# Kernel optimization log

Measured on AMD Instinct MI355X. Metric: run time of the kernel, lower is better.

Reference implementation:

```python
import jax, jax.numpy as jnp
import numpy as np

EMB = 128     # embedding_size
HEADS = 4     # n_heads
LAYERS = 2    # n_layers
T = 10        # number of graphs / timesteps (== window_size)
N = 20000     # nodes per graph
E = 320000    # edges per graph
B = 4096      # clf_nodes
WIN = 10      # window_size
NEG_SLOPE = 0.2


def setup_inputs() -> dict:
    key = jax.random.key(0)
    ks = jax.random.split(key, 26)
    p = lambda k, shape: 0.05 * jax.random.normal(k, shape, jnp.float32)
    inp = {
        "embeddings": jax.random.normal(ks[0], (T, N, EMB), jnp.float32),
        "edges": jax.random.randint(ks[1], (T, 2, E), 0, N),
        "node_type": jax.random.randint(ks[2], (T, N), 0, 4),
        "edge_type": jax.random.randint(ks[3], (T, E), 0, 4),
        "clf_neighbors": jax.random.randint(ks[4], (B,), 0, N),
        "clf_nodes": jax.random.randint(ks[5], (B,), 0, N),
        # branch 1 GAT stacks: lin weight [L, H*C, D], attention vecs [L, H, C], bias [L, H*C]
        "gat_W1": p(ks[6], (LAYERS, HEADS * EMB, EMB)),
        "gat_as1": p(ks[7], (LAYERS, HEADS, EMB)),
        "gat_ad1": p(ks[8], (LAYERS, HEADS, EMB)),
        "gat_b1": p(ks[9], (LAYERS, HEADS * EMB)),
        "lin_W1": p(ks[10], (LAYERS, EMB, HEADS * EMB)),
        "lin_b1": p(ks[11], (LAYERS, EMB)),
        # branch 2
        "gat_W2": p(ks[12], (LAYERS, HEADS * EMB, EMB)),
        "gat_as2": p(ks[13], (LAYERS, HEADS, EMB)),
        "gat_ad2": p(ks[14], (LAYERS, HEADS, EMB)),
        "gat_b2": p(ks[15], (LAYERS, HEADS * EMB)),
        "lin_W2": p(ks[16], (LAYERS, EMB, HEADS * EMB)),
        "lin_b2": p(ks[17], (LAYERS, EMB)),
        # head MLP (fc1 consumes flattened [window * 2*D])
        "fc1_W": p(ks[18], (EMB, 2 * EMB * WIN)),
        "fc1_b": p(ks[19], (EMB,)),
        "fc2_W": p(ks[20], (2, EMB)),
        "fc2_b": p(ks[21], (2,)),
    }
    return inp


def _gat(x, src, dst, W, a_s, a_d, b):
    """PyG-style GATConv (concat=True, self-loops already in src/dst, eval mode)."""
    n = x.shape[0]
    h = (x @ W.T).reshape(n, HEADS, EMB)                       # [N,H,C]
    logits = jax.nn.leaky_relu((h * a_s).sum(-1)[src] + (h * a_d).sum(-1)[dst], NEG_SLOPE)  # [Etot,H]
    logits = logits - jax.ops.segment_max(logits, dst, num_segments=n)[dst]
    ex = jnp.exp(logits)
    alpha = ex / jax.ops.segment_sum(ex, dst, num_segments=n)[dst]  # segment softmax over targets
    out = jax.ops.segment_sum(alpha[:, :, None] * h[src], dst, num_segments=n)  # [N,H,C]
    return out.reshape(n, HEADS * EMB) + b


def _branch(embeddings, edges, gW, gas, gad, gb, lW, lb):
    loops = jnp.arange(N)

    def step(carry, inputs):
        x, edge = inputs
        src = jnp.concatenate([edge[0], loops])  # add self loops (PyG default)
        dst = jnp.concatenate([edge[1], loops])
        for i in range(LAYERS):
            x = _gat(x, src, dst, gW[i], gas[i], gad[i], gb[i])
            x = jax.nn.relu(x @ lW[i].T + lb[i])
        return carry, x

    _, outs = jax.lax.scan(step, 0, (embeddings, edges))
    return outs  # [T,N,EMB]


def reference(embeddings, edges, node_type, edge_type, clf_neighbors, clf_nodes,
              gat_W1, gat_as1, gat_ad1, gat_b1, lin_W1, lin_b1,
              gat_W2, gat_as2, gat_ad2, gat_b2, lin_W2, lin_b2,
              fc1_W, fc1_b, fc2_W, fc2_b):
    o1 = _branch(embeddings, edges, gat_W1, gat_as1, gat_ad1, gat_b1, lin_W1, lin_b1)
    o2 = _branch(embeddings, edges, gat_W2, gat_as2, gat_ad2, gat_b2, lin_W2, lin_b2)
    # original prepends each graph's output -> reversed timestep order
    e1 = o1[::-1][:, clf_nodes].transpose(1, 0, 2)  # [B,T,EMB]
    e2 = o2[::-1][:, clf_nodes].transpose(1, 0, 2)
    temp = jnp.concatenate([e1, e2], axis=2)        # [B,T,2*EMB]
    # slen == window_size -> skip buffer is fully filled by temp
    flat = temp.reshape(temp.shape[0], WIN * 2 * EMB)
    h = jax.nn.relu(flat @ fc1_W.T + fc1_b)
    return jax.nn.relu(h @ fc2_W.T + fc2_b)        # [B,2]
```

## Files before the change

kernel.cpp:

```cpp
#include <hip/hip_runtime.h>
#include <cstdint>

#define NNODES 20000
#define NEDGES 320000
#define ETOT   340000
#define TSTEPS 10
#define BCLF   4096
#define EMB    128
#define HC     512
#define NEG_SLOPE 0.2f

#define NSB    64
#define SBSPAN 313
#define PCAP   6912
#define ECHUNK 2048
#define NCHUNKS ((NEDGES + ECHUNK - 1) / ECHUNK)
#define NSCHUNK ((NNODES + 255) / 256)
#define STAGECAP 7424

typedef _Float16 half_t;
typedef __attribute__((ext_vector_type(8))) _Float16 half8;
typedef __attribute__((ext_vector_type(4))) float floatx4;

__global__ void cvt_split_kernel(const float* __restrict__ in,
                                 half_t* __restrict__ hi, half_t* __restrict__ lo, long n4) {
    long i = (long)blockIdx.x * 256 + threadIdx.x;
    if (i >= n4) return;
    float4 v = *(const float4*)&in[i * 4];
    half_t h[4], l[4];
    h[0] = (half_t)v.x; l[0] = (half_t)(v.x - (float)h[0]);
    h[1] = (half_t)v.y; l[1] = (half_t)(v.y - (float)h[1]);
    h[2] = (half_t)v.z; l[2] = (half_t)(v.z - (float)h[2]);
    h[3] = (half_t)v.w; l[3] = (half_t)(v.w - (float)h[3]);
    *(unsigned long long*)&hi[i * 4] = *(unsigned long long*)h;
    *(unsigned long long*)&lo[i * 4] = *(unsigned long long*)l;
}

__global__ __launch_bounds__(256) void part64_kernel(const int* __restrict__ edges,
                                                     int* __restrict__ bcnt,
                                                     int* __restrict__ pairs) {
    int g = blockIdx.y;
    int c = blockIdx.x;
    __shared__ int hist[NSB], gbase[NSB], cur[NSB];
    if (threadIdx.x < NSB) hist[threadIdx.x] = 0;
    __syncthreads();
    const int* srcp = edges + (long)g * 2 * NEDGES;
    const int* dstp = srcp + NEDGES;
    int e0 = c * ECHUNK + threadIdx.x;
    int s[8], d[8], sb[8];
#pragma unroll
    for (int i = 0; i < 8; i++) {
        int e = e0 + i * 256;
        if (e < NEDGES) {
            s[i] = srcp[e];
            d[i] = dstp[e];
            sb[i] = (int)((unsigned)d[i] / (unsigned)SBSPAN);
            atomicAdd(&hist[sb[i]], 1);
        } else sb[i] = -1;
    }
    __syncthreads();
    if (threadIdx.x < NSB) {
        int h = hist[threadIdx.x];
        gbase[threadIdx.x] = h ? atomicAdd(&bcnt[g * NSB + threadIdx.x], h) : 0;
        cur[threadIdx.x] = 0;
    }
    __syncthreads();
#pragma unroll
    for (int i = 0; i < 8; i++) {
        if (sb[i] >= 0) {
            int pos = gbase[sb[i]] + atomicAdd(&cur[sb[i]], 1);
            int v = s[i] | ((d[i] - sb[i] * SBSPAN) << 15);
            pairs[((long)(g * NSB + sb[i])) * PCAP + pos] = v;
        }
    }
}

__global__ __launch_bounds__(256) void count_sb_kernel(const int* __restrict__ pairs,
                                                       const int* __restrict__ bcnt,
                                                       int* __restrict__ counts) {
    int g = blockIdx.x >> 6, sb = blockIdx.x & 63;
    __shared__ int hist[SBSPAN];
    for (int i = threadIdx.x; i < SBSPAN; i += 256) hist[i] = 0;
    __syncthreads();
    int n0 = sb * SBSPAN;
    int cnt = bcnt[g * NSB + sb];
    const int* p = pairs + (long)(g * NSB + sb) * PCAP;
    for (int k = threadIdx.x; k < cnt; k += 256)
        atomicAdd(&hist[p[k] >> 15], 1);
    __syncthreads();
    int nn = min(SBSPAN, NNODES - n0);
    for (int i = threadIdx.x; i < nn; i += 256)
        counts[g * NNODES + n0 + i] = hist[i];
}

__global__ void scanA_kernel(const int* __restrict__ counts, int* __restrict__ bsum) {
    int g = blockIdx.x / NSCHUNK, ch = blockIdx.x % NSCHUNK;
    int i = ch * 256 + threadIdx.x;
    int v = (i < NNODES) ? counts[g * NNODES + i] + 1 : 0;
    for (int off = 32; off; off >>= 1) v += __shfl_down(v, off);
    __shared__ int ws[4];
    if ((threadIdx.x & 63) == 0) ws[threadIdx.x >> 6] = v;
    __syncthreads();
    if (threadIdx.x == 0) bsum[blockIdx.x] = ws[0] + ws[1] + ws[2] + ws[3];
}

__global__ void scanB_kernel(const int* __restrict__ bsum, int* __restrict__ boff,
                             int* __restrict__ rowptr) {
    int g = blockIdx.x;
    int tid = threadIdx.x;
    int v = (tid < NSCHUNK) ? bsum[g * NSCHUNK + tid] : 0;
    __shared__ int buf[128];
    buf[tid] = v;
    __syncthreads();
    for (int off = 1; off < 128; off <<= 1) {
        int t = (tid >= off) ? buf[tid - off] : 0;
        __syncthreads();
        buf[tid] += t;
        __syncthreads();
    }
    if (tid < NSCHUNK) boff[g * NSCHUNK + tid] = buf[tid] - v;
    if (tid == 127) rowptr[g * (NNODES + 1) + NNODES] = buf[127];
}

__global__ void scanC_kernel(const int* __restrict__ counts, const int* __restrict__ boff,
                             int* __restrict__ rowptr) {
    int g = blockIdx.x / NSCHUNK, ch = blockIdx.x % NSCHUNK;
    int tid = threadIdx.x;
    int i = ch * 256 + tid;
    int v = (i < NNODES) ? counts[g * NNODES + i] + 1 : 0;
    __shared__ int buf[256];
    buf[tid] = v;
    __syncthreads();
    for (int off = 1; off < 256; off <<= 1) {
        int t = (tid >= off) ? buf[tid - off] : 0;
        __syncthreads();
        buf[tid] += t;
        __syncthreads();
    }
    int excl = boff[blockIdx.x] + buf[tid] - v;
    if (i < NNODES) rowptr[g * (NNODES + 1) + i] = excl;
}

__global__ __launch_bounds__(256) void fill_sb_kernel(const int* __restrict__ pairs,
                                                      const int* __restrict__ bcnt,
                                                      const int* __restrict__ rowptr,
                                                      int* __restrict__ csr_src) {
    int g = blockIdx.x >> 6, sb = blockIdx.x & 63;
    __shared__ int cur[SBSPAN];
    __shared__ int stage[STAGECAP];
    int n0 = sb * SBSPAN;
    int nn = min(SBSPAN, NNODES - n0);
    const int* rp = rowptr + g * (NNODES + 1);
    int base = rp[n0];
    int span = rp[n0 + nn] - base;
    for (int i = threadIdx.x; i < nn; i += 256) {
        int rb = rp[n0 + i] - base;
        stage[rb] = n0 + i;
        cur[i] = rb + 1;
    }
    __syncthreads();
    int cnt = bcnt[g * NSB + sb];
    const int* p = pairs + (long)(g * NSB + sb) * PCAP;
    for (int k = threadIdx.x; k < cnt; k += 256) {
        int v = p[k];
        int pos = atomicAdd(&cur[v >> 15], 1);
        stage[pos] = v & 0x7fff;
    }
    __syncthreads();
    int* dst = csr_src + (long)g * ETOT + base;
    for (int k = threadIdx.x; k < span; k += 256) dst[k] = stage[k];
}

__global__ void prep_was_kernel(const float* __restrict__ W1, const float* __restrict__ W2,
                                const float* __restrict__ as1, const float* __restrict__ as2,
                                const float* __restrict__ ad1, const float* __restrict__ ad2,
                                float* __restrict__ was, float* __restrict__ wad) {
    int b = blockIdx.x;
    int l = b >> 3, z = (b >> 2) & 1, h = b & 3;
    int k = threadIdx.x;
    const float* W  = z ? W2 : W1;
    const float* av = z ? as2 : as1;
    const float* dv = z ? ad2 : ad1;
    float s = 0.f, d = 0.f;
    for (int c = 0; c < 128; c++) {
        float w = W[(long)l * HC * EMB + (h * 128 + c) * 128 + k];
        s = fmaf(w, av[(l * 4 + h) * 128 + c], s);
        d = fmaf(w, dv[(l * 4 + h) * 128 + c], d);
    }
    long idx = ((l * 2 + z) * 4 + h) * 128 + k;
    was[idx] = s;
    wad[idx] = d;
}

__global__ void pack_ws_kernel(const float* __restrict__ wasb, const float* __restrict__ wadb,
                               half_t* __restrict__ WS0h, half_t* __restrict__ WS0l,
                               half_t* __restrict__ WS1h, half_t* __restrict__ WS1l) {
    int b = blockIdx.x;
    int k = threadIdx.x;
    if (b < 16) {
        int z = b >> 3, d = (b >> 2) & 1, h = b & 3;
        const float* src = d ? wadb : wasb;
        float v = src[((long)z * 4 + h) * 128 + k];
        half_t hi = (half_t)v;
        WS0h[b * 128 + k] = hi;
        WS0l[b * 128 + k] = (half_t)(v - (float)hi);
    } else {
        int b2 = b - 16;
        int z = b2 >> 4, r = b2 & 15;
        float v = 0.f;
        if (r < 8) {
            int d = r >> 2, h = r & 3;
            const float* src = d ? wadb : wasb;
            v = src[((long)(2 + z) * 4 + h) * 128 + k];
        }
        half_t hi = (half_t)v;
        WS1h[(z * 16 + r) * 128 + k] = hi;
        WS1l[(z * 16 + r) * 128 + k] = (half_t)(v - (float)hi);
    }
}

__global__ void prep_M_kernel(const float* __restrict__ gW1, const float* __restrict__ gW2,
                              const float* __restrict__ lW1, const float* __restrict__ lW2,
                              half_t* __restrict__ Mh, half_t* __restrict__ Ml) {
    int k = blockIdx.x;
    int inst = blockIdx.y;
    int l = inst >> 1, z = inst & 1;
    int c = threadIdx.x;
    const float* gW = (z ? gW2 : gW1) + (long)l * HC * EMB;
    const float* lW = (z ? lW2 : lW1) + (long)l * EMB * HC;
    float acc[4] = {0.f, 0.f, 0.f, 0.f};
    for (int cp = 0; cp < 128; cp++) {
#pragma unroll
        for (int h = 0; h < 4; h++) {
            float lw = lW[(long)k * 512 + h * 128 + cp];
            float gw = gW[(long)(h * 128 + cp) * 128 + c];
            acc[h] = fmaf(lw, gw, acc[h]);
        }
    }
#pragma unroll
    for (int h = 0; h < 4; h++) {
        long o = ((long)inst * 128 + k) * 512 + h * 128 + c;
        half_t hi = (half_t)acc[h];
        Mh[o] = hi;
        Ml[o] = (half_t)(acc[h] - (float)hi);
    }
}

__global__ void prep_cb_kernel(const float* __restrict__ lW1, const float* __restrict__ lW2,
                               const float* __restrict__ gb1_, const float* __restrict__ gb2_,
                               const float* __restrict__ lb1_, const float* __restrict__ lb2_,
                               float* __restrict__ cb) {
    int inst = blockIdx.x;
    int l = inst >> 1, z = inst & 1;
    int k = threadIdx.x;
    const float* lW = (z ? lW2 : lW1) + (long)l * EMB * HC;
    const float* gb = (z ? gb2_ : gb1_) + l * HC;
    const float* lb = (z ? lb2_ : lb1_) + l * EMB;
    float a = lb[k];
    for (int j = 0; j < 512; j++) a = fmaf(lW[(long)k * 512 + j], gb[j], a);
    cb[inst * 128 + k] = a;
}

__global__ __launch_bounds__(256) void scores_b(
    const half_t* __restrict__ Ahb, const half_t* __restrict__ Alb, long aInst,
    const half_t* __restrict__ WShb, const half_t* __restrict__ WSlb, long wInst, int wMask,
    float* __restrict__ outb, long oInst, int M, int OS, int CMAX) {
    int iy = blockIdx.y;
    const half_t* Ah = Ahb + (long)iy * aInst;
    const half_t* Al = Alb + (long)iy * aInst;
    const half_t* WSh = WShb + (long)(iy & wMask) * wInst;
    const half_t* WSl = WSlb + (long)(iy & wMask) * wInst;
    float* out = outb + (long)iy * oInst;
    __shared__ half_t Bh[16 * 128];
    __shared__ half_t Bl[16 * 128];
    int tid = threadIdx.x;
    *(half8*)&Bh[tid * 8] = *(const half8*)&WSh[tid * 8];
    *(half8*)&Bl[tid * 8] = *(const half8*)&WSl[tid * 8];
    __syncthreads();
    int wave = tid >> 6, lane = tid & 63;
    int l16 = lane & 15, chunk = lane >> 4;
    int r0 = blockIdx.x * 64 + wave * 16;
    int rowc = r0 + l16; if (rowc > M - 1) rowc = M - 1;
    floatx4 acc = (floatx4)0.f;
#pragma unroll
    for (int ko = 0; ko < 128; ko += 32) {
        half8 ah = *(const half8*)&Ah[(long)rowc * 128 + ko + chunk * 8];
        half8 al = *(const half8*)&Al[(long)rowc * 128 + ko + chunk * 8];
        half8 bh = *(const half8*)&Bh[l16 * 128 + ko + chunk * 8];
        half8 bl = *(const half8*)&Bl[l16 * 128 + ko + chunk * 8];
        acc = __builtin_amdgcn_mfma_f32_16x16x32_f16(ah, bh, acc, 0, 0, 0);
        acc = __builtin_amdgcn_mfma_f32_16x16x32_f16(ah, bl, acc, 0, 0, 0);
        acc = __builtin_amdgcn_mfma_f32_16x16x32_f16(al, bh, acc, 0, 0, 0);
    }
#pragma unroll
    for (int reg = 0; reg < 4; reg++) {
        int rr = r0 + chunk * 4 + reg;
        if (rr < M && l16 < CMAX) out[(long)rr * OS + l16] = acc[reg];
    }
}

__global__ __launch_bounds__(256) void agg_x_kernel(
    const half_t* __restrict__ Xb, long xsT, long xsG,
    const float* __restrict__ ssb, int stsh, long ssT, long ssG, int zcol,
    const int* __restrict__ rowptr, const int* __restrict__ csr_src,
    half_t* __restrict__ Yh, half_t* __restrict__ Yl, int t0) {
    int tz = blockIdx.z, t = t0 + tz, z = blockIdx.y;
    int gz = tz * 2 + z;
    int n = blockIdx.x * 4 + (threadIdx.x >> 6);
    int lane = threadIdx.x & 63;
    int h = lane >> 4, cg = lane & 15;
    const int* rp = rowptr + t * (NNODES + 1);
    int beg = rp[n], end = rp[n + 1];
    const int* cs = csr_src + (long)t * ETOT;
    const half_t* Xz = Xb + (long)t * xsT + (long)gz * xsG;
    const float* sz = ssb + (long)t * ssT + (long)gz * ssG + (long)z * zcol;
    float sd = sz[((long)n << stsh) + 4 + h];
    float acc[8];
#pragma unroll
    for (int c = 0; c < 8; c++) acc[c] = 0.f;
    float den = 0.f;
    int j = beg;
    for (; j + 4 <= end; j += 4) {
        int s0 = cs[j], s1 = cs[j + 1], s2 = cs[j + 2], s3 = cs[j + 3];
        float v0 = sz[((long)s0 << stsh) + h];
        float v1 = sz[((long)s1 << stsh) + h];
        float v2 = sz[((long)s2 << stsh) + h];
        float v3 = sz[((long)s3 << stsh) + h];
        half8 x0 = *(const half8*)&Xz[(long)s0 * 128 + cg * 8];
        half8 x1 = *(const half8*)&Xz[(long)s1 * 128 + cg * 8];
        half8 x2 = *(const half8*)&Xz[(long)s2 * 128 + cg * 8];
        half8 x3 = *(const half8*)&Xz[(long)s3 * 128 + cg * 8];
        float L0 = v0 + sd, L1 = v1 + sd, L2 = v2 + sd, L3 = v3 + sd;
        float w0 = __expf(fmaxf(L0, NEG_SLOPE * L0));
        float w1 = __expf(fmaxf(L1, NEG_SLOPE * L1));
        float w2 = __expf(fmaxf(L2, NEG_SLOPE * L2));
        float w3 = __expf(fmaxf(L3, NEG_SLOPE * L3));
        den += (w0 + w1) + (w2 + w3);
#pragma unroll
        for (int c = 0; c < 8; c++) {
            float a = acc[c];
            a = fmaf(w0, (float)x0[c], a);
            a = fmaf(w1, (float)x1[c], a);
            a = fmaf(w2, (float)x2[c], a);
            a = fmaf(w3, (float)x3[c], a);
            acc[c] = a;
        }
    }
    for (; j < end; j++) {
        int src = cs[j];
        float sv = sz[((long)src << stsh) + h];
        half8 x = *(const half8*)&Xz[(long)src * 128 + cg * 8];
        float L = sv + sd;
        float w = __expf(fmaxf(L, NEG_SLOPE * L));
        den += w;
#pragma unroll
        for (int c = 0; c < 8; c++) acc[c] = fmaf(w, (float)x[c], acc[c]);
    }
    float inv = 1.0f / den;
    half8 oh, ol;
#pragma unroll
    for (int c = 0; c < 8; c++) {
        float v = acc[c] * inv;
        half_t hi = (half_t)v;
        oh[c] = hi;
        ol[c] = (half_t)(v - (float)hi);
    }
    long yb = ((long)gz * NNODES + n) * 512 + h * 128 + cg * 8;
    *(half8*)&Yh[yb] = oh;
    *(half8*)&Yl[yb] = ol;
}

template <bool F32OUT>
__global__ __launch_bounds__(256) void gemm_b(
    const half_t* __restrict__ Ahb, const half_t* __restrict__ Alb, long aInst,
    const half_t* __restrict__ Bhb, const half_t* __restrict__ Blb, long bInst,
    const float* __restrict__ biasb, long biasInst,
    half_t* __restrict__ Ch, half_t* __restrict__ Cl, float* __restrict__ Cf,
    long cInst, int M, int N, int K) {
    const int i = blockIdx.z;
    const half_t* __restrict__ Ah = Ahb + (long)i * aInst;
    const half_t* __restrict__ Al = Alb + (long)i * aInst;
    const half_t* __restrict__ Bh = Bhb + (long)(i & 1) * bInst;
    const half_t* __restrict__ Bl = Blb + (long)(i & 1) * bInst;
    const float* __restrict__ bias = biasb + (long)(i & 1) * biasInst;

    __shared__ half_t Ash[4 * 128 * 8];
    __shared__ half_t Asl[4 * 128 * 8];
    __shared__ half_t Bsh[4 * 128 * 8];
    __shared__ half_t Bsl[4 * 128 * 8];

    const int tid = threadIdx.x;
    const int row0 = blockIdx.x * 128;
    const int col0 = blockIdx.y * 128;
    const int wave = tid >> 6;
    const int lane = tid & 63;
    const int wm = (wave >> 1) * 64;
    const int wn = (wave & 1) * 64;
    const int chunk = lane >> 4;
    const int l16 = lane & 15;

    floatx4 acc[4][4];
#pragma unroll
    for (int ii = 0; ii < 4; ii++)
#pragma unroll
        for (int j = 0; j < 4; j++) acc[ii][j] = (floatx4)0.0f;

    for (int k0 = 0; k0 < K; k0 += 32) {
        __syncthreads();
#pragma unroll
        for (int p = 0; p < 2; p++) {
            int idx = p * 256 + tid;
            int r = idx >> 2, kc = idx & 3;
            int arow = row0 + r;
            half8 vah, val;
            if (arow < M) {
                vah = *(const half8*)&Ah[(long)arow * K + k0 + kc * 8];
                val = *(const half8*)&Al[(long)arow * K + k0 + kc * 8];
            } else {
#pragma unroll
                for (int q = 0; q < 8; q++) { vah[q] = (half_t)0.f; val[q] = (half_t)0.f; }
            }
            *(half8*)&Ash[(kc * 128 + r) * 8] = vah;
            *(half8*)&Asl[(kc * 128 + r) * 8] = val;
            long boff = (long)(col0 + r) * K + k0 + kc * 8;
            *(half8*)&Bsh[(kc * 128 + r) * 8] = *(const half8*)&Bh[boff];
            *(half8*)&Bsl[(kc * 128 + r) * 8] = *(const half8*)&Bl[boff];
        }
        __syncthreads();
        half8 afh[4], afl[4], bfh[4], bfl[4];
#pragma unroll
        for (int mi = 0; mi < 4; mi++) {
            int o = (chunk * 128 + wm + mi * 16 + l16) * 8;
            afh[mi] = *(const half8*)&Ash[o];
            afl[mi] = *(const half8*)&Asl[o];
        }
#pragma unroll
        for (int ni = 0; ni < 4; ni++) {
            int o = (chunk * 128 + wn + ni * 16 + l16) * 8;
            bfh[ni] = *(const half8*)&Bsh[o];
            bfl[ni] = *(const half8*)&Bsl[o];
        }
#pragma unroll
        for (int mi = 0; mi < 4; mi++)
#pragma unroll
            for (int ni = 0; ni < 4; ni++) {
                acc[mi][ni] = __builtin_amdgcn_mfma_f32_16x16x32_f16(
                    afh[mi], bfh[ni], acc[mi][ni], 0, 0, 0);
                acc[mi][ni] = __builtin_amdgcn_mfma_f32_16x16x32_f16(
                    afh[mi], bfl[ni], acc[mi][ni], 0, 0, 0);
                acc[mi][ni] = __builtin_amdgcn_mfma_f32_16x16x32_f16(
                    afl[mi], bfh[ni], acc[mi][ni], 0, 0, 0);
            }
    }

    const int r4 = (lane >> 4) * 4;
#pragma unroll
    for (int mi = 0; mi < 4; mi++) {
#pragma unroll
        for (int reg = 0; reg < 4; reg++) {
            int row = row0 + wm + mi * 16 + r4 + reg;
            if (row >= M) continue;
#pragma unroll
            for (int ni = 0; ni < 4; ni++) {
                int col = col0 + wn + ni * 16 + l16;
                float v = fmaxf(acc[mi][ni][reg] + bias[col], 0.f);
                long o = (long)i * cInst + (long)row * N + col;
                if (F32OUT) {
                    Cf[o] = v;
                } else {
                    half_t hi = (half_t)v;
                    Ch[o] = hi;
                    Cl[o] = (half_t)(v - (float)hi);
                }
            }
        }
    }
}

__global__ void gather_kernel(const half_t* __restrict__ Xh, const half_t* __restrict__ Xl,
                              const int* __restrict__ clf,
                              half_t* __restrict__ flath, half_t* __restrict__ flatl, int t0) {
    int b = blockIdx.x;
    int z = blockIdx.y;
    int tz = blockIdx.z;
    int t = t0 + tz, gz = tz * 2 + z;
    int j = threadIdx.x;
    int node = clf[b];
    long dst = (long)b * (TSTEPS * 2 * EMB) + (TSTEPS - 1 - t) * (2 * EMB) + z * EMB;
    long src = ((long)gz * NNODES + node) * EMB;
    ((unsigned int*)&flath[dst])[j] = ((const unsigned int*)&Xh[src])[j];
    ((unsigned int*)&flatl[dst])[j] = ((const unsigned int*)&Xl[src])[j];
}

__global__ void fc2_kernel(const float* __restrict__ h1, const float* __restrict__ W,
                           const float* __restrict__ bias, float* __restrict__ out) {
    int row = blockIdx.x;
    int lane = threadIdx.x;
    float x0 = h1[(long)row * 128 + lane];
    float x1 = h1[(long)row * 128 + 64 + lane];
    float p0 = x0 * W[lane] + x1 * W[64 + lane];
    float p1 = x0 * W[128 + lane] + x1 * W[192 + lane];
    for (int off = 32; off; off >>= 1) {
        p0 += __shfl_down(p0, off);
        p1 += __shfl_down(p1, off);
    }
    if (lane == 0) {
        out[row * 2 + 0] = fmaxf(p0 + bias[0], 0.f);
        out[row * 2 + 1] = fmaxf(p1 + bias[1], 0.f);
    }
}

extern "C" void kernel_launch(void* const* d_in, const int* in_sizes, int n_in,
                              void* d_out, int out_size, void* d_ws, size_t ws_size,
                              hipStream_t stream) {
    const float* emb     = (const float*)d_in[0];
    const int*   edges   = (const int*)d_in[1];
    const int*   clf     = (const int*)d_in[5];
    const float* gat_W1  = (const float*)d_in[6];
    const float* gat_as1 = (const float*)d_in[7];
    const float* gat_ad1 = (const float*)d_in[8];
    const float* gat_b1  = (const float*)d_in[9];
    const float* lin_W1  = (const float*)d_in[10];
    const float* lin_b1  = (const float*)d_in[11];
    const float* gat_W2  = (const float*)d_in[12];
    const float* gat_as2 = (const float*)d_in[13];
    const float* gat_ad2 = (const float*)d_in[14];
    const float* gat_b2  = (const float*)d_in[15];
    const float* lin_W2  = (const float*)d_in[16];
    const float* lin_b2  = (const float*)d_in[17];
    const float* fc1_W   = (const float*)d_in[18];
    const float* fc1_b   = (const float*)d_in[19];
    const float* fc2_W   = (const float*)d_in[20];
    const float* fc2_b   = (const float*)d_in[21];
    float* out = (float*)d_out;

    char* ws = (char*)d_ws;
    size_t off = 0;
    auto alloc = [&](size_t bytes) -> char* {
        char* p = ws + off;
        off += (bytes + 255) & ~(size_t)255;
        return p;
    };
    int* counts  = (int*)alloc((size_t)TSTEPS * NNODES * 4);
    int* rowptr  = (int*)alloc((size_t)TSTEPS * (NNODES + 1) * 4);
    int* csr_src = (int*)alloc((size_t)TSTEPS * ETOT * 4);
    int* bsum    = (int*)alloc((size_t)TSTEPS * NSCHUNK * 4);
    int* boff    = (int*)alloc((size_t)TSTEPS * NSCHUNK * 4);
    int* bcnt    = (int*)alloc((size_t)TSTEPS * NSB * 4);
    half_t* embh = (half_t*)alloc((size_t)TSTEPS * NNODES * EMB * 2);
    half_t* Mh   = (half_t*)alloc((size_t)4 * EMB * HC * 2);
    half_t* Ml   = (half_t*)alloc((size_t)4 * EMB * HC * 2);
    float*  cb   = (float*)alloc((size_t)4 * EMB * 4);
    half_t* fc1Wh = (half_t*)alloc((size_t)EMB * 2 * EMB * TSTEPS * 2);
    half_t* fc1Wl = (half_t*)alloc((size_t)EMB * 2 * EMB * TSTEPS * 2);
    float* wasb = (float*)alloc((size_t)2 * 2 * 4 * 128 * 4);
    float* wadb = (float*)alloc((size_t)2 * 2 * 4 * 128 * 4);
    half_t* WS0h = (half_t*)alloc((size_t)16 * 128 * 2);
    half_t* WS0l = (half_t*)alloc((size_t)16 * 128 * 2);
    half_t* WS1h = (half_t*)alloc((size_t)2 * 16 * 128 * 2);
    half_t* WS1l = (half_t*)alloc((size_t)2 * 16 * 128 * 2);
    float* s0buf = (float*)alloc((size_t)TSTEPS * NNODES * 16 * 4);
    half_t* flath = (half_t*)alloc((size_t)BCLF * (TSTEPS * 2 * EMB) * 2);
    half_t* flatl = (half_t*)alloc((size_t)BCLF * (TSTEPS * 2 * EMB) * 2);
    float* h1buf = (float*)alloc((size_t)BCLF * EMB * 4);

    size_t region_base = off;
    half_t* embl = (half_t*)alloc((size_t)TSTEPS * NNODES * EMB * 2);
    int* pairs   = (int*)alloc((size_t)TSTEPS * NSB * PCAP * 4);

    const size_t perT = ((size_t)2 * NNODES * HC * 2 * 2) +
                        ((size_t)2 * NNODES * EMB * 2 * 2) +
                        ((size_t)2 * NNODES * 8 * 4) + 2048;
    int TG = 1;
    if (ws_size > region_base + perT) {
        size_t cap = (ws_size - region_base) / perT;
        TG = (cap >= 10) ? 10 : (int)cap;
        if (TG < 1) TG = 1;
    }
    off = region_base;
    half_t* Yh = (half_t*)alloc((size_t)TG * 2 * NNODES * HC * 2);
    half_t* Yl = (half_t*)alloc((size_t)TG * 2 * NNODES * HC * 2);
    half_t* Xh = (half_t*)alloc((size_t)TG * 2 * NNODES * EMB * 2);
    half_t* Xl = (half_t*)alloc((size_t)TG * 2 * NNODES * EMB * 2);
    float* s1buf = (float*)alloc((size_t)TG * 2 * NNODES * 8 * 4);

    {
        long n4 = (long)TSTEPS * NNODES * EMB / 4;
        cvt_split_kernel<<<(int)((n4 + 255) / 256), 256, 0, stream>>>(emb, embh, embl, n4);
        long f4 = (long)EMB * 2 * EMB * TSTEPS / 4;
        cvt_split_kernel<<<(int)((f4 + 255) / 256), 256, 0, stream>>>(fc1_W, fc1Wh, fc1Wl, f4);
    }
    prep_was_kernel<<<16, 128, 0, stream>>>(gat_W1, gat_W2, gat_as1, gat_as2,
                                            gat_ad1, gat_ad2, wasb, wadb);
    pack_ws_kernel<<<48, 128, 0, stream>>>(wasb, wadb, WS0h, WS0l, WS1h, WS1l);
    prep_M_kernel<<<dim3(128, 4), 128, 0, stream>>>(gat_W1, gat_W2, lin_W1, lin_W2, Mh, Ml);
    prep_cb_kernel<<<4, 128, 0, stream>>>(lin_W1, lin_W2, gat_b1, gat_b2, lin_b1, lin_b2, cb);

    scores_b<<<dim3(3125, 1), 256, 0, stream>>>(
        embh, embl, 0, WS0h, WS0l, 0, 0, s0buf, 0, TSTEPS * NNODES, 16, 16);

    hipMemsetAsync(bcnt, 0, (size_t)TSTEPS * NSB * 4, stream);
    part64_kernel<<<dim3(NCHUNKS, TSTEPS), 256, 0, stream>>>(edges, bcnt, pairs);
    count_sb_kernel<<<NSB * TSTEPS, 256, 0, stream>>>(pairs, bcnt, counts);
    scanA_kernel<<<TSTEPS * NSCHUNK, 256, 0, stream>>>(counts, bsum);
    scanB_kernel<<<TSTEPS, 128, 0, stream>>>(bsum, boff, rowptr);
    scanC_kernel<<<TSTEPS * NSCHUNK, 256, 0, stream>>>(counts, boff, rowptr);
    fill_sb_kernel<<<NSB * TSTEPS, 256, 0, stream>>>(pairs, bcnt, rowptr, csr_src);

    for (int t0 = 0; t0 < TSTEPS; t0 += TG) {
        int tg = (TSTEPS - t0 < TG) ? (TSTEPS - t0) : TG;
        agg_x_kernel<<<dim3(5000, 2, tg), 256, 0, stream>>>(
            embh, (long)NNODES * EMB, 0L,
            s0buf, 4, (long)NNODES * 16, 0L, 8,
            rowptr, csr_src, Yh, Yl, t0);
        gemm_b<false><<<dim3(157, 1, 2 * tg), 256, 0, stream>>>(
            Yh, Yl, (long)NNODES * HC,
            Mh, Ml, (long)EMB * HC, cb, EMB,
            Xh, Xl, nullptr, (long)NNODES * EMB, NNODES, EMB, HC);
        scores_b<<<dim3(313, 2 * tg), 256, 0, stream>>>(
            Xh, Xl, (long)NNODES * EMB,
            WS1h, WS1l, (long)16 * 128, 1,
            s1buf, (long)NNODES * 8, NNODES, 8, 8);
        agg_x_kernel<<<dim3(5000, 2, tg), 256, 0, stream>>>(
            Xh, 0L, (long)NNODES * EMB,
            s1buf, 3, 0L, (long)NNODES * 8, 0,
            rowptr, csr_src, Yh, Yl, t0);
        gemm_b<false><<<dim3(157, 1, 2 * tg), 256, 0, stream>>>(
            Yh, Yl, (long)NNODES * HC,
            Mh + (long)2 * EMB * HC, Ml + (long)2 * EMB * HC, (long)EMB * HC,
            cb + 2 * EMB, EMB,
            Xh, Xl, nullptr, (long)NNODES * EMB, NNODES, EMB, HC);
        gather_kernel<<<dim3(BCLF, 2, tg), 64, 0, stream>>>(Xh, Xl, clf, flath, flatl, t0);
    }
    gemm_b<true><<<dim3(32, 1, 1), 256, 0, stream>>>(
        flath, flatl, 0, fc1Wh, fc1Wl, 0, fc1_b, 0,
        nullptr, nullptr, h1buf, 0, BCLF, EMB, TSTEPS * 2 * EMB);
    fc2_kernel<<<BCLF, 64, 0, stream>>>(h1buf, fc2_W, fc2_b, out);
}
```

Baseline: 1.887 ms.

## Split-K the fc1 GEMM and prefetch CSR indices in aggregation loop

```diff
diff --git a/kernel.cpp b/kernel.cpp
--- a/kernel.cpp
+++ b/kernel.cpp
@@ -319,9 +319,8 @@
 #pragma unroll
     for (int c = 0; c < 8; c++) acc[c] = 0.f;
     float den = 0.f;
-    int j = beg;
-    for (; j + 4 <= end; j += 4) {
-        int s0 = cs[j], s1 = cs[j + 1], s2 = cs[j + 2], s3 = cs[j + 3];
+
+    auto proc4 = [&](int s0, int s1, int s2, int s3) {
         float v0 = sz[((long)s0 << stsh) + h];
         float v1 = sz[((long)s1 << stsh) + h];
         float v2 = sz[((long)s2 << stsh) + h];
@@ -345,6 +344,23 @@
             a = fmaf(w3, (float)x3[c], a);
             acc[c] = a;
         }
+    };
+
+    int j = beg;
+    int rem = end - beg;
+    if (rem >= 8) {
+        int a0 = cs[j], a1 = cs[j + 1], a2 = cs[j + 2], a3 = cs[j + 3];
+        while (j + 8 <= end) {
+            int b0 = cs[j + 4], b1 = cs[j + 5], b2 = cs[j + 6], b3 = cs[j + 7];
+            proc4(a0, a1, a2, a3);
+            a0 = b0; a1 = b1; a2 = b2; a3 = b3;
+            j += 4;
+        }
+        proc4(a0, a1, a2, a3);
+        j += 4;
+    } else if (rem >= 4) {
+        proc4(cs[j], cs[j + 1], cs[j + 2], cs[j + 3]);
+        j += 4;
     }
     for (; j < end; j++) {
         int src = cs[j];
@@ -370,12 +386,11 @@
     *(half8*)&Yl[yb] = ol;
 }
 
-template <bool F32OUT>
 __global__ __launch_bounds__(256) void gemm_b(
     const half_t* __restrict__ Ahb, const half_t* __restrict__ Alb, long aInst,
     const half_t* __restrict__ Bhb, const half_t* __restrict__ Blb, long bInst,
     const float* __restrict__ biasb, long biasInst,
-    half_t* __restrict__ Ch, half_t* __restrict__ Cl, float* __restrict__ Cf,
+    half_t* __restrict__ Ch, half_t* __restrict__ Cl,
     long cInst, int M, int N, int K) {
     const int i = blockIdx.z;
     const half_t* __restrict__ Ah = Ahb + (long)i * aInst;
@@ -465,16 +480,103 @@
                 int col = col0 + wn + ni * 16 + l16;
                 float v = fmaxf(acc[mi][ni][reg] + bias[col], 0.f);
                 long o = (long)i * cInst + (long)row * N + col;
-                if (F32OUT) {
-                    Cf[o] = v;
-                } else {
-                    half_t hi = (half_t)v;
-                    Ch[o] = hi;
-                    Cl[o] = (half_t)(v - (float)hi);
-                }
+                half_t hi = (half_t)v;
+                Ch[o] = hi;
+                Cl[o] = (half_t)(v - (float)hi);
             }
         }
     }
+}
+
+__global__ __launch_bounds__(256) void fc1_part_kernel(
+    const half_t* __restrict__ Ah, const half_t* __restrict__ Al,
+    const half_t* __restrict__ Bh, const half_t* __restrict__ Bl,
+    float* __restrict__ pbuf, int M, int N, int K, int kslice) {
+    const int ks = blockIdx.y;
+    const int kbeg = ks * kslice;
+    const int kend = kbeg + kslice;
+
+    __shared__ half_t Ash[4 * 128 * 8];
+    __shared__ half_t Asl[4 * 128 * 8];
+    __shared__ half_t Bsh[4 * 128 * 8];
+    __shared__ half_t Bsl[4 * 128 * 8];
+
+    const int tid = threadIdx.x;
+    const int row0 = blockIdx.x * 128;
+    const int wave = tid >> 6;
+    const int lane = tid & 63;
+    const int wm = (wave >> 1) * 64;
+    const int wn = (wave & 1) * 64;
+    const int chunk = lane >> 4;
+    const int l16 = lane & 15;
+
+    floatx4 acc[4][4];
+#pragma unroll
+    for (int ii = 0; ii < 4; ii++)
+#pragma unroll
+        for (int j = 0; j < 4; j++) acc[ii][j] = (floatx4)0.0f;
+
+    for (int k0 = kbeg; k0 < kend; k0 += 32) {
+        __syncthreads();
+#pragma unroll
+        for (int p = 0; p < 2; p++) {
+            int idx = p * 256 + tid;
+            int r = idx >> 2, kc = idx & 3;
+            long aoff = (long)(row0 + r) * K + k0 + kc * 8;
+            *(half8*)&Ash[(kc * 128 + r) * 8] = *(const half8*)&Ah[aoff];
+            *(half8*)&Asl[(kc * 128 + r) * 8] = *(const half8*)&Al[aoff];
+            long boff = (long)r * K + k0 + kc * 8;
+            *(half8*)&Bsh[(kc * 128 + r) * 8] = *(const half8*)&Bh[boff];
+            *(half8*)&Bsl[(kc * 128 + r) * 8] = *(const half8*)&Bl[boff];
+        }
+        __syncthreads();
+        half8 afh[4], afl[4], bfh[4], bfl[4];
+#pragma unroll
+        for (int mi = 0; mi < 4; mi++) {
+            int o = (chunk * 128 + wm + mi * 16 + l16) * 8;
+            afh[mi] = *(const half8*)&Ash[o];
+            afl[mi] = *(const half8*)&Asl[o];
+        }
+#pragma unroll
+        for (int ni = 0; ni < 4; ni++) {
+            int o = (chunk * 128 + wn + ni * 16 + l16) * 8;
+            bfh[ni] = *(const half8*)&Bsh[o];
+            bfl[ni] = *(const half8*)&Bsl[o];
+        }
+#pragma unroll
+        for (int mi = 0; mi < 4; mi++)
+#pragma unroll
+            for (int ni = 0; ni < 4; ni++) {
+                acc[mi][ni] = __builtin_amdgcn_mfma_f32_16x16x32_f16(
+                    afh[mi], bfh[ni], acc[mi][ni], 0, 0, 0);
+                acc[mi][ni] = __builtin_amdgcn_mfma_f32_16x16x32_f16(
+                    afh[mi], bfl[ni], acc[mi][ni], 0, 0, 0);
+                acc[mi][ni] = __builtin_amdgcn_mfma_f32_16x16x32_f16(
+                    afl[mi], bfh[ni], acc[mi][ni], 0, 0, 0);
+            }
+    }
+
+    const int r4 = (lane >> 4) * 4;
+#pragma unroll
+    for (int mi = 0; mi < 4; mi++)
+#pragma unroll
+        for (int reg = 0; reg < 4; reg++) {
+            int row = row0 + wm + mi * 16 + r4 + reg;
+#pragma unroll
+            for (int ni = 0; ni < 4; ni++) {
+                int col = wn + ni * 16 + l16;
+                pbuf[((long)ks * M + row) * N + col] = acc[mi][ni][reg];
+            }
+        }
+}
+
+__global__ void fc1_reduce_kernel(const float* __restrict__ pbuf, const float* __restrict__ bias,
+                                  float* __restrict__ h1, int MN, int KS) {
+    int i = blockIdx.x * 256 + threadIdx.x;
+    if (i >= MN) return;
+    float a = 0.f;
+    for (int ks = 0; ks < KS; ks++) a += pbuf[(long)ks * MN + i];
+    h1[i] = fmaxf(a + bias[i & (EMB - 1)], 0.f);
 }
 
 __global__ void gather_kernel(const half_t* __restrict__ Xh, const half_t* __restrict__ Xl,
@@ -613,10 +715,10 @@
             embh, (long)NNODES * EMB, 0L,
             s0buf, 4, (long)NNODES * 16, 0L, 8,
             rowptr, csr_src, Yh, Yl, t0);
-        gemm_b<false><<<dim3(157, 1, 2 * tg), 256, 0, stream>>>(
+        gemm_b<<<dim3(157, 1, 2 * tg), 256, 0, stream>>>(
             Yh, Yl, (long)NNODES * HC,
             Mh, Ml, (long)EMB * HC, cb, EMB,
-            Xh, Xl, nullptr, (long)NNODES * EMB, NNODES, EMB, HC);
+            Xh, Xl, (long)NNODES * EMB, NNODES, EMB, HC);
         scores_b<<<dim3(313, 2 * tg), 256, 0, stream>>>(
             Xh, Xl, (long)NNODES * EMB,
             WS1h, WS1l, (long)16 * 128, 1,
@@ -625,15 +727,17 @@
             Xh, 0L, (long)NNODES * EMB,
             s1buf, 3, 0L, (long)NNODES * 8, 0,
             rowptr, csr_src, Yh, Yl, t0);
-        gemm_b<false><<<dim3(157, 1, 2 * tg), 256, 0, stream>>>(
+        gemm_b<<<dim3(157, 1, 2 * tg), 256, 0, stream>>>(
             Yh, Yl, (long)NNODES * HC,
             Mh + (long)2 * EMB * HC, Ml + (long)2 * EMB * HC, (long)EMB * HC,
             cb + 2 * EMB, EMB,
-            Xh, Xl, nullptr, (long)NNODES * EMB, NNODES, EMB, HC);
+            Xh, Xl, (long)NNODES * EMB, NNODES, EMB, HC);
         gather_kernel<<<dim3(BCLF, 2, tg), 64, 0, stream>>>(Xh, Xl, clf, flath, flatl, t0);
     }
-    gemm_b<true><<<dim3(32, 1, 1), 256, 0, stream>>>(
-        flath, flatl, 0, fc1Wh, fc1Wl, 0, fc1_b, 0,
-        nullptr, nullptr, h1buf, 0, BCLF, EMB, TSTEPS * 2 * EMB);
+    float* pbuf = (float*)Yh;
+    fc1_part_kernel<<<dim3(32, 8), 256, 0, stream>>>(
+        flath, flatl, fc1Wh, fc1Wl, pbuf, BCLF, EMB, TSTEPS * 2 * EMB, (TSTEPS * 2 * EMB) / 8);
+    fc1_reduce_kernel<<<(BCLF * EMB + 255) / 256, 256, 0, stream>>>(
+        pbuf, fc1_b, h1buf, BCLF * EMB, 8);
     fc2_kernel<<<BCLF, 64, 0, stream>>>(h1buf, fc2_W, fc2_b, out);
 }
```

Result: faster. 1.770 ms (-6.2%).
